# Performance work log

Hardware: AMD Instinct MI355X
Metric: run time of the kernel (lower is better)

Reference implementation:

```python
import jax, jax.numpy as jnp
import numpy as np

B, S, E = 2, 2048, 2048
H, G = 32, 8          # n_heads, n_groups
D = E // H            # head_dim = 64


def setup_inputs() -> dict:
    key = jax.random.key(0)
    ks = jax.random.split(key, 5)
    scale = 1.0 / np.sqrt(E)
    return {
        "X": jax.random.normal(ks[0], (B, S, E), dtype=jnp.float32),
        "Wq": jax.random.normal(ks[1], (E, E), dtype=jnp.float32) * scale,
        "Wk": jax.random.normal(ks[2], (E, G * D), dtype=jnp.float32) * scale,
        "Wv": jax.random.normal(ks[3], (E, G * D), dtype=jnp.float32) * scale,
        "Wo": jax.random.normal(ks[4], (E, E), dtype=jnp.float32) * scale,
    }


def reference(X, Wq, Wk, Wv, Wo):
    b, s, e = X.shape
    # projections
    q = (X @ Wq).reshape(b, s, H, D).transpose(0, 2, 1, 3)      # [B,H,S,D]
    k = (X @ Wk).reshape(b, s, G, D).transpose(0, 2, 1, 3)      # [B,G,S,D]
    v = (X @ Wv).reshape(b, s, G, D).transpose(0, 2, 1, 3)      # [B,G,S,D]
    # torch view(B, H//G, G, S, D): head h -> (a=h//G, g=h%G)
    q = q.reshape(b, H // G, G, s, D)                           # [B,A,G,S,D]
    scores = jnp.einsum('bagsd,bgtd->bagst', q, k) / np.sqrt(D) # [B,A,G,S,S]
    causal = jnp.tril(jnp.ones((s, s), dtype=bool))
    scores = jnp.where(causal, scores, -jnp.inf)
    probs = jax.nn.softmax(scores, axis=-1)
    out = jnp.einsum('bagst,bgtd->bagsd', probs, v)             # [B,A,G,S,D]
    out = out.reshape(b, H, s, D).transpose(0, 2, 1, 3).reshape(b, s, e)
    return out @ Wo
```

## Files before the change

kernel.cpp:

```cpp
#include <hip/hip_runtime.h>
#include <hip/hip_bf16.h>

typedef unsigned short u16;
typedef __bf16 bf16x8 __attribute__((ext_vector_type(8)));
typedef float f32x4 __attribute__((ext_vector_type(4)));
typedef unsigned short u16x4 __attribute__((ext_vector_type(4)));

#define MFMA16(a, b, c) __builtin_amdgcn_mfma_f32_16x16x32_bf16(a, b, c, 0, 0, 0)

__device__ __forceinline__ u16 f2bf(float f) {
  union { float f; unsigned u; } v; v.f = f;
  unsigned r = v.u + 0x7FFFu + ((v.u >> 16) & 1u);
  return (u16)(r >> 16);
}

__device__ __forceinline__ u16 f2bf_native(float f) {
  __hip_bfloat16 hb = __float2bfloat16(f);
  u16 out;
  __builtin_memcpy(&out, &hb, 2);
  return out;
}

__device__ __forceinline__ void gload16(const u16* g, u16* l) {
  __builtin_amdgcn_global_load_lds(
      (const __attribute__((address_space(1))) unsigned int*)g,
      (__attribute__((address_space(3))) unsigned int*)l, 16, 0, 0);
}

__global__ void cvt_x(const float* __restrict__ X, u16* __restrict__ Xb, int n4) {
  int i = blockIdx.x * blockDim.x + threadIdx.x;
  if (i < n4) {
    float4 v = ((const float4*)X)[i];
    u16x4 o = { f2bf(v.x), f2bf(v.y), f2bf(v.z), f2bf(v.w) };
    ((u16x4*)Xb)[i] = o;
  }
}

__global__ void transpose_cvt(const float* __restrict__ W, u16* __restrict__ WT, int K, int N) {
  __shared__ float t[32][33];
  int n0 = blockIdx.x * 32, k0 = blockIdx.y * 32;
  int tx = threadIdx.x, ty = threadIdx.y;
  t[ty][tx] = W[(size_t)(k0 + ty) * N + n0 + tx];
  __syncthreads();
  WT[(size_t)(n0 + ty) * K + k0 + tx] = f2bf(t[tx][ty]);
}

__device__ __forceinline__ void stage_tile(const u16* __restrict__ A, const u16* __restrict__ BT,
                                           u16* la, u16* lb, int bm, int bn, int K, int k0, int tid) {
  {
    int arow = tid >> 2;
    int ac = (tid & 3) ^ ((arow >> 1) & 3);
    gload16(A + (size_t)(bm + arow) * K + k0 + ac * 8, la + tid * 8);
  }
#pragma unroll
  for (int i = 0; i < 2; ++i) {
    int s = i * 512 + tid;
    int brow = s >> 2;
    int bc = (s & 3) ^ ((brow >> 1) & 3);
    gload16(BT + (size_t)(bn + brow) * K + k0 + bc * 8, lb + s * 8);
  }
}

template <int STORE>
__global__ __launch_bounds__(512) void gemm8(const u16* __restrict__ A,
                                             const u16* __restrict__ BT,
                                             void* __restrict__ Cv,
                                             int M, int N, int K) {
  __shared__ u16 lA[2][128 * 32];
  __shared__ u16 lB[2][256 * 32];
  const int tid = threadIdx.x;
  const int lane = tid & 63, wave = tid >> 6;
  const int gx = gridDim.x;
  const int nwg = gx * gridDim.y;
  const int bid = blockIdx.y * gx + blockIdx.x;
  const int sw = (bid & 7) * (nwg >> 3) + (bid >> 3);
  const int bx = sw % gx, by = sw / gx;
  const int bm = by * 128, bn = bx * 256;
  const int wm = (wave >> 2) * 64, wn = (wave & 3) * 64;
  const int l15 = lane & 15, l4 = lane >> 4;

  f32x4 acc[4][4] = {};

  u16* ra = (u16*)lA[0]; u16* rb = (u16*)lB[0];
  u16* wa = (u16*)lA[1]; u16* wb = (u16*)lB[1];

  stage_tile(A, BT, ra, rb, bm, bn, K, 0, tid);
  asm volatile("s_waitcnt vmcnt(0)" ::: "memory");
  __builtin_amdgcn_s_barrier();

  const int NT = K >> 5;
#pragma unroll 1
  for (int t = 0; t < NT; ++t) {
    if (t + 1 < NT) stage_tile(A, BT, wa, wb, bm, bn, K, (t + 1) << 5, tid);
    bf16x8 af[4], bf[4];
#pragma unroll
    for (int i = 0; i < 4; ++i) {
      int r = wm + i * 16 + l15;
      af[i] = *(const bf16x8*)&ra[r * 32 + (l4 ^ ((r >> 1) & 3)) * 8];
      int n = wn + i * 16 + l15;
      bf[i] = *(const bf16x8*)&rb[n * 32 + (l4 ^ ((n >> 1) & 3)) * 8];
    }
    __builtin_amdgcn_s_setprio(1);
#pragma unroll
    for (int i = 0; i < 4; ++i)
#pragma unroll
      for (int j = 0; j < 4; ++j)
        acc[i][j] = MFMA16(af[i], bf[j], acc[i][j]);
    __builtin_amdgcn_s_setprio(0);
    asm volatile("s_waitcnt vmcnt(0)" ::: "memory");
    __builtin_amdgcn_s_barrier();
    u16* t1 = ra; ra = wa; wa = t1;
    u16* t2 = rb; rb = wb; wb = t2;
  }

#pragma unroll
  for (int i = 0; i < 4; ++i) {
    int row = bm + wm + i * 16 + l4 * 4;
#pragma unroll
    for (int j = 0; j < 4; ++j) {
      int col = bn + wn + j * 16 + l15;
#pragma unroll
      for (int e = 0; e < 4; ++e) {
        float v = acc[i][j][e];
        if (STORE == 2) {
          ((float*)Cv)[(size_t)(row + e) * N + col] = v;
        } else {
          u16* Qb = (u16*)Cv;
          u16* Kb = Qb + 8388608;
          u16* Vt = Kb + 2097152;
          if (col < 2048)       Qb[(size_t)(row + e) * 2048 + col] = f2bf(v * 0.125f);
          else if (col < 2560)  Kb[(size_t)(row + e) * 512 + (col - 2048)] = f2bf(v);
          else                  Vt[(size_t)(col - 2560) * 4096 + (row + e)] = f2bf(v);
        }
      }
    }
  }
}

__global__ __launch_bounds__(512) void attn_fwd(const u16* __restrict__ Q,
                                                const u16* __restrict__ Kb,
                                                const u16* __restrict__ VT,
                                                u16* __restrict__ AO) {
  const int pair = blockIdx.x, g = blockIdx.y, b = blockIdx.z;
  const int tid = threadIdx.x;
  const int lane = tid & 63;
  const int wave = tid >> 6;
  const int a = wave >> 1;
  const int h = a * 8 + g;
  const int l15 = lane & 15, l4 = lane >> 4;

  __shared__ u16 Klds[2][64 * 64];
  __shared__ u16 Vlds[2][64 * 64];
  __shared__ u16 Plds[8][16 * 64];

  const int srow = tid >> 3, sc = (tid & 7) ^ (srow & 7);

  int cur = 0;
#pragma unroll 1
  for (int pass = 0; pass < 2; ++pass) {
    const int qt = (pass == 0) ? pair : 63 - pair;
    const int qw0 = qt * 32 + (wave & 1) * 16;
    const int nt = qt / 2 + 1;

    const u16* qp = Q + (size_t)(b * 2048 + qw0 + l15) * 2048 + h * 64 + l4 * 8;
    bf16x8 qf0 = *(const bf16x8*)qp;
    bf16x8 qf1 = *(const bf16x8*)(qp + 32);

    float m_r = -1e30f, l_r = 0.f;
    f32x4 o[4] = {};

    {
      gload16(Kb + (size_t)(b * 2048 + 0 + srow) * 512 + g * 64 + sc * 8, &Klds[cur][tid * 8]);
      gload16(VT + (size_t)(g * 64 + srow) * 4096 + b * 2048 + 0 + sc * 8, &Vlds[cur][tid * 8]);
      asm volatile("s_waitcnt vmcnt(0)" ::: "memory");
      __builtin_amdgcn_s_barrier();
    }

#pragma unroll 1
    for (int ti = 0; ti < nt; ++ti) {
      const int t0 = ti * 64;
      if (ti + 1 < nt) {
        const int tn = t0 + 64;
        gload16(Kb + (size_t)(b * 2048 + tn + srow) * 512 + g * 64 + sc * 8, &Klds[cur ^ 1][tid * 8]);
        gload16(VT + (size_t)(g * 64 + srow) * 4096 + b * 2048 + tn + sc * 8, &Vlds[cur ^ 1][tid * 8]);
      }

      if (t0 <= qw0 + 15) {
        const u16* Kc = Klds[cur];
        const u16* Vc = Vlds[cur];
        f32x4 s[4];
        __builtin_amdgcn_s_setprio(1);
#pragma unroll
        for (int ct = 0; ct < 4; ++ct) {
          int t = ct * 16 + l15;
          bf16x8 kf0 = *(const bf16x8*)&Kc[(t * 8 + (l4 ^ (t & 7))) * 8];
          bf16x8 kf1 = *(const bf16x8*)&Kc[(t * 8 + ((l4 + 4) ^ (t & 7))) * 8];
          f32x4 sv = {0.f, 0.f, 0.f, 0.f};
          sv = MFMA16(kf0, qf0, sv);
          sv = MFMA16(kf1, qf1, sv);
          s[ct] = sv;
        }
        __builtin_amdgcn_s_setprio(0);

        if (t0 + 63 > qw0) {
          const int qg = qw0 + l15;
#pragma unroll
          for (int ct = 0; ct < 4; ++ct)
#pragma unroll
            for (int e = 0; e < 4; ++e) {
              int tg = t0 + ct * 16 + l4 * 4 + e;
              if (tg > qg) s[ct][e] = -1e30f;
            }
        }

        float m0 = fmaxf(fmaxf(s[0][0], s[0][1]), fmaxf(s[0][2], s[0][3]));
        float m1 = fmaxf(fmaxf(s[1][0], s[1][1]), fmaxf(s[1][2], s[1][3]));
        float m2 = fmaxf(fmaxf(s[2][0], s[2][1]), fmaxf(s[2][2], s[2][3]));
        float m3 = fmaxf(fmaxf(s[3][0], s[3][1]), fmaxf(s[3][2], s[3][3]));
        float mt = fmaxf(fmaxf(m0, m1), fmaxf(m2, m3));
        mt = fmaxf(mt, __shfl_xor(mt, 16));
        mt = fmaxf(mt, __shfl_xor(mt, 32));

        if (!__all(mt <= m_r + 8.0f)) {
          float mn = fmaxf(m_r, mt);
          float alpha = __expf(m_r - mn);
          m_r = mn;
          l_r *= alpha;
#pragma unroll
          for (int e = 0; e < 4; ++e) {
            float ae = __shfl(alpha, l4 * 4 + e);
            o[0][e] *= ae; o[1][e] *= ae; o[2][e] *= ae; o[3][e] *= ae;
          }
        }

        u16* P = Plds[wave];
        float rs = 0.f;
#pragma unroll
        for (int ct = 0; ct < 4; ++ct) {
          u16x4 pk;
#pragma unroll
          for (int e = 0; e < 4; ++e) {
            float p = __expf(s[ct][e] - m_r);
            rs += p;
            pk[e] = f2bf_native(p);
          }
          int slot = (ct * 2 + (l4 >> 1)) ^ (l15 & 7);
          *(u16x4*)&P[l15 * 64 + slot * 8 + (l4 & 1) * 4] = pk;
        }
        rs += __shfl_xor(rs, 16);
        rs += __shfl_xor(rs, 32);
        l_r += rs;

        __builtin_amdgcn_s_setprio(1);
#pragma unroll
        for (int kk = 0; kk < 2; ++kk) {
          bf16x8 pf = *(const bf16x8*)&P[l15 * 64 + (((kk * 4 + l4) ^ (l15 & 7)) * 8)];
#pragma unroll
          for (int cd = 0; cd < 4; ++cd) {
            int d = cd * 16 + l15;
            bf16x8 vf = *(const bf16x8*)&Vc[(d * 8 + ((kk * 4 + l4) ^ (d & 7))) * 8];
            o[cd] = MFMA16(pf, vf, o[cd]);
          }
        }
        __builtin_amdgcn_s_setprio(0);
      }

      asm volatile("s_waitcnt vmcnt(0)" ::: "memory");
      __builtin_amdgcn_s_barrier();
      cur ^= 1;
    }

    float rli = 1.0f / l_r;
#pragma unroll
    for (int cd = 0; cd < 4; ++cd)
#pragma unroll
      for (int e = 0; e < 4; ++e) {
        float rle = __shfl(rli, l4 * 4 + e);
        int r = l4 * 4 + e;
        int d = cd * 16 + l15;
        AO[(size_t)(b * 2048 + qw0 + r) * 2048 + h * 64 + d] = f2bf_native(o[cd][e] * rle);
      }
  }
}

extern "C" void kernel_launch(void* const* d_in, const int* in_sizes, int n_in,
                              void* d_out, int out_size, void* d_ws, size_t ws_size,
                              hipStream_t stream) {
  const float* X  = (const float*)d_in[0];
  const float* Wq = (const float*)d_in[1];
  const float* Wk = (const float*)d_in[2];
  const float* Wv = (const float*)d_in[3];
  const float* Wo = (const float*)d_in[4];
  float* out = (float*)d_out;

  u16* ws  = (u16*)d_ws;
  u16* Xb  = ws;
  u16* WqT = Xb  + 8388608;
  u16* WkT = WqT + 4194304;
  u16* WvT = WkT + 1048576;
  u16* WoT = WvT + 1048576;
  u16* Qb  = WoT + 4194304;
  u16* Kbf = Qb  + 8388608;
  u16* VTb = Kbf + 2097152;
  u16* AOb = Xb;

  cvt_x<<<8192, 256, 0, stream>>>(X, Xb, 2097152);
  dim3 tb(32, 32);
  transpose_cvt<<<dim3(64, 64), tb, 0, stream>>>(Wq, WqT, 2048, 2048);
  transpose_cvt<<<dim3(16, 64), tb, 0, stream>>>(Wk, WkT, 2048, 512);
  transpose_cvt<<<dim3(16, 64), tb, 0, stream>>>(Wv, WvT, 2048, 512);
  transpose_cvt<<<dim3(64, 64), tb, 0, stream>>>(Wo, WoT, 2048, 2048);

  gemm8<4><<<dim3(12, 32), 512, 0, stream>>>(Xb, WqT, Qb, 4096, 3072, 2048);

  attn_fwd<<<dim3(32, 8, 2), 512, 0, stream>>>(Qb, Kbf, VTb, AOb);

  gemm8<2><<<dim3(8, 32), 512, 0, stream>>>(AOb, WoT, out, 4096, 2048, 2048);
}
```

Measured before the change: 225.5 us.

## Enlarge GEMM tiles to 256x256x64 with phased prefetch interleaving

Replaces the 128x256x32 GEMM with a 256x256 tile and a K-step of 64, giving each wave a 128x64 output. Next-tile staging is split into halves and issued during the first two of four compute phases. The LDS swizzle moves to an 8-chunk XOR pattern. This raises data reuse per block, but halves the grid size (128 and 192 blocks) and increases register and LDS pressure, which may leave CUs idle.

```diff
diff --git a/kernel.cpp b/kernel.cpp
--- a/kernel.cpp
+++ b/kernel.cpp
@@ -45,29 +45,26 @@
   WT[(size_t)(n0 + ty) * K + k0 + tx] = f2bf(t[tx][ty]);
 }
 
-__device__ __forceinline__ void stage_tile(const u16* __restrict__ A, const u16* __restrict__ BT,
-                                           u16* la, u16* lb, int bm, int bn, int K, int k0, int tid) {
-  {
-    int arow = tid >> 2;
-    int ac = (tid & 3) ^ ((arow >> 1) & 3);
-    gload16(A + (size_t)(bm + arow) * K + k0 + ac * 8, la + tid * 8);
-  }
+__device__ __forceinline__ void stage_half256(const u16* __restrict__ A, const u16* __restrict__ BT,
+                                              u16* la, u16* lb, int bm, int bn, int K, int k0,
+                                              int tid, int half) {
 #pragma unroll
   for (int i = 0; i < 2; ++i) {
-    int s = i * 512 + tid;
-    int brow = s >> 2;
-    int bc = (s & 3) ^ ((brow >> 1) & 3);
-    gload16(BT + (size_t)(bn + brow) * K + k0 + bc * 8, lb + s * 8);
+    int s = half * 1024 + i * 512 + tid;
+    int row = s >> 3;
+    int c = (s & 7) ^ (row & 7);
+    gload16(A + (size_t)(bm + row) * K + k0 + c * 8, la + s * 8);
+    gload16(BT + (size_t)(bn + row) * K + k0 + c * 8, lb + s * 8);
   }
 }
 
 template <int STORE>
-__global__ __launch_bounds__(512) void gemm8(const u16* __restrict__ A,
-                                             const u16* __restrict__ BT,
-                                             void* __restrict__ Cv,
-                                             int M, int N, int K) {
-  __shared__ u16 lA[2][128 * 32];
-  __shared__ u16 lB[2][256 * 32];
+__global__ __launch_bounds__(512) void gemm256(const u16* __restrict__ A,
+                                               const u16* __restrict__ BT,
+                                               void* __restrict__ Cv,
+                                               int M, int N, int K) {
+  __shared__ u16 lA[2][256 * 64];
+  __shared__ u16 lB[2][256 * 64];
   const int tid = threadIdx.x;
   const int lane = tid & 63, wave = tid >> 6;
   const int gx = gridDim.x;
@@ -75,50 +72,72 @@
   const int bid = blockIdx.y * gx + blockIdx.x;
   const int sw = (bid & 7) * (nwg >> 3) + (bid >> 3);
   const int bx = sw % gx, by = sw / gx;
-  const int bm = by * 128, bn = bx * 256;
-  const int wm = (wave >> 2) * 64, wn = (wave & 3) * 64;
+  const int bm = by * 256, bn = bx * 256;
+  const int wr = wave >> 2, wc = wave & 3;
   const int l15 = lane & 15, l4 = lane >> 4;
 
-  f32x4 acc[4][4] = {};
-
-  u16* ra = (u16*)lA[0]; u16* rb = (u16*)lB[0];
-  u16* wa = (u16*)lA[1]; u16* wb = (u16*)lB[1];
-
-  stage_tile(A, BT, ra, rb, bm, bn, K, 0, tid);
+  f32x4 acc[8][4] = {};
+
+  stage_half256(A, BT, lA[0], lB[0], bm, bn, K, 0, tid, 0);
+  stage_half256(A, BT, lA[0], lB[0], bm, bn, K, 0, tid, 1);
   asm volatile("s_waitcnt vmcnt(0)" ::: "memory");
   __builtin_amdgcn_s_barrier();
 
-  const int NT = K >> 5;
+  const int NT = K >> 6;
 #pragma unroll 1
   for (int t = 0; t < NT; ++t) {
-    if (t + 1 < NT) stage_tile(A, BT, wa, wb, bm, bn, K, (t + 1) << 5, tid);
-    bf16x8 af[4], bf[4];
-#pragma unroll
-    for (int i = 0; i < 4; ++i) {
-      int r = wm + i * 16 + l15;
-      af[i] = *(const bf16x8*)&ra[r * 32 + (l4 ^ ((r >> 1) & 3)) * 8];
-      int n = wn + i * 16 + l15;
-      bf[i] = *(const bf16x8*)&rb[n * 32 + (l4 ^ ((n >> 1) & 3)) * 8];
+    const u16* Ar = lA[t & 1];
+    const u16* Br = lB[t & 1];
+    u16* Aw = lA[(t + 1) & 1];
+    u16* Bw = lB[(t + 1) & 1];
+    bf16x8 bfr[4][2];
+#pragma unroll
+    for (int p = 0; p < 4; ++p) {
+      if (p == 0) {
+#pragma unroll
+        for (int j = 0; j < 4; ++j) {
+          int n = wc * 64 + j * 16 + l15;
+#pragma unroll
+          for (int kk = 0; kk < 2; ++kk) {
+            int c = (kk * 4 + l4) ^ (n & 7);
+            bfr[j][kk] = *(const bf16x8*)&Br[(n * 8 + c) * 8];
+          }
+        }
+      }
+      bf16x8 af[2][2];
+#pragma unroll
+      for (int i16 = 0; i16 < 2; ++i16) {
+        int r = wr * 128 + p * 32 + i16 * 16 + l15;
+#pragma unroll
+        for (int kk = 0; kk < 2; ++kk) {
+          int c = (kk * 4 + l4) ^ (r & 7);
+          af[i16][kk] = *(const bf16x8*)&Ar[(r * 8 + c) * 8];
+        }
+      }
+      if (p < 2 && t + 1 < NT)
+        stage_half256(A, BT, Aw, Bw, bm, bn, K, (t + 1) << 6, tid, p);
+
+      __builtin_amdgcn_s_barrier();
+      __builtin_amdgcn_s_setprio(1);
+#pragma unroll
+      for (int i16 = 0; i16 < 2; ++i16)
+#pragma unroll
+        for (int j = 0; j < 4; ++j)
+#pragma unroll
+          for (int kk = 0; kk < 2; ++kk)
+            acc[p * 2 + i16][j] = MFMA16(af[i16][kk], bfr[j][kk], acc[p * 2 + i16][j]);
+      __builtin_amdgcn_s_setprio(0);
+      if (p == 3) asm volatile("s_waitcnt vmcnt(0)" ::: "memory");
+      __builtin_amdgcn_s_barrier();
     }
-    __builtin_amdgcn_s_setprio(1);
-#pragma unroll
-    for (int i = 0; i < 4; ++i)
-#pragma unroll
-      for (int j = 0; j < 4; ++j)
-        acc[i][j] = MFMA16(af[i], bf[j], acc[i][j]);
-    __builtin_amdgcn_s_setprio(0);
-    asm volatile("s_waitcnt vmcnt(0)" ::: "memory");
-    __builtin_amdgcn_s_barrier();
-    u16* t1 = ra; ra = wa; wa = t1;
-    u16* t2 = rb; rb = wb; wb = t2;
-  }
-
-#pragma unroll
-  for (int i = 0; i < 4; ++i) {
-    int row = bm + wm + i * 16 + l4 * 4;
+  }
+
+#pragma unroll
+  for (int i = 0; i < 8; ++i) {
+    int row = bm + wr * 128 + i * 16 + l4 * 4;
 #pragma unroll
     for (int j = 0; j < 4; ++j) {
-      int col = bn + wn + j * 16 + l15;
+      int col = bn + wc * 64 + j * 16 + l15;
 #pragma unroll
       for (int e = 0; e < 4; ++e) {
         float v = acc[i][j][e];
@@ -311,9 +330,9 @@
   transpose_cvt<<<dim3(16, 64), tb, 0, stream>>>(Wv, WvT, 2048, 512);
   transpose_cvt<<<dim3(64, 64), tb, 0, stream>>>(Wo, WoT, 2048, 2048);
 
-  gemm8<4><<<dim3(12, 32), 512, 0, stream>>>(Xb, WqT, Qb, 4096, 3072, 2048);
+  gemm256<4><<<dim3(12, 16), 512, 0, stream>>>(Xb, WqT, Qb, 4096, 3072, 2048);
 
   attn_fwd<<<dim3(32, 8, 2), 512, 0, stream>>>(Qb, Kbf, VTb, AOb);
 
-  gemm8<2><<<dim3(8, 32), 512, 0, stream>>>(AOb, WoT, out, 4096, 2048, 2048);
-}
+  gemm256<2><<<dim3(8, 16), 512, 0, stream>>>(AOb, WoT, out, 4096, 2048, 2048);
+}
```

Measured after the change: 234.1 us. 1.04x slower.
